# Kernel optimization log

Hardware: AMD Instinct MI355X
Metric: run time of the kernel (lower is better)

## Reference

```python
import jax, jax.numpy as jnp
import numpy as np

B, T, U, V = 4, 300, 80, 1024
DE, DD, INNER = 320, 320, 512


def setup_inputs() -> dict:
    key = jax.random.key(0)
    ks = jax.random.split(key, 6)
    enc_state = jax.random.normal(ks[0], (B, T, DE), jnp.float32)
    dec_state = jax.random.normal(ks[1], (B, U + 1, DD), jnp.float32)
    Wf = jax.random.normal(ks[2], (INNER, DE + DD), jnp.float32) / np.float32(np.sqrt(DE + DD))
    bf = jnp.zeros((INNER,), jnp.float32)
    Wp = jax.random.normal(ks[3], (V, INNER), jnp.float32) / np.float32(np.sqrt(INNER))
    bp = jnp.zeros((V,), jnp.float32)
    targets = jax.random.randint(ks[4], (B, U), 1, V).astype(jnp.int32)  # labels avoid blank=0
    inputs_length = jnp.full((B,), T, jnp.int32)
    targets_length = jnp.full((B,), U, jnp.int32)
    return {"enc_state": enc_state, "dec_state": dec_state, "Wf": Wf, "bf": bf,
            "Wp": Wp, "bp": bp, "targets": targets,
            "inputs_length": inputs_length, "targets_length": targets_length}


def joint_logits(enc, dec, Wf, bf, Wp, bp):
    # Linear over concat([enc, dec]) == Linear(enc) + Linear(dec): avoids materializing the concat.
    de = enc.shape[-1]
    Wf_e, Wf_d = Wf[:, :de], Wf[:, de:]
    enc_p = jnp.einsum('btd,id->bti', enc, Wf_e)   # [B,T,inner]
    dec_p = jnp.einsum('bud,id->bui', dec, Wf_d)   # [B,U1,inner]
    h = jnp.tanh(enc_p[:, :, None, :] + dec_p[:, None, :, :] + bf)  # [B,T,U1,inner]
    return jnp.einsum('btui,vi->btuv', h, Wp) + bp  # [B,T,U1,V]


def rnnt_loss(log_probs, targets, t_len, u_len):
    # log_probs: [B,T,U1,V], blank index 0.
    lp_blank = log_probs[..., 0]  # [B,T,U1]
    lp_emit = jnp.take_along_axis(log_probs[:, :, :-1, :], targets[:, None, :, None], axis=3)[..., 0]  # [B,T,U]
    # row0: alpha[0,u] = sum_{k<u} emit[0,k]
    row0 = jnp.pad(jnp.cumsum(lp_emit[:, 0, :], axis=-1), ((0, 0), (1, 0)))  # [B,U1]

    def outer(alpha_prev, xs):
        blank_prev, emit_cur = xs  # [B,U1], [B,U]
        first = alpha_prev[:, 0] + blank_prev[:, 0]  # [B]

        def inner(c, x):
            a_plus_b, e = x  # [B],[B]
            c2 = jnp.logaddexp(a_plus_b, c + e)
            return c2, c2
        xs_in = ((alpha_prev[:, 1:] + blank_prev[:, 1:]).T, emit_cur.T)  # [U,B]
        _, rest = jax.lax.scan(inner, first, xs_in)  # [U,B]
        row = jnp.concatenate([first[None, :], rest], axis=0).T  # [B,U1]
        return row, row

    xs = (jnp.swapaxes(lp_blank[:, :-1, :], 0, 1), jnp.swapaxes(lp_emit[:, 1:, :], 0, 1))
    _, rows = jax.lax.scan(outer, row0, xs)  # [T-1,B,U1]
    alpha = jnp.concatenate([row0[None], rows], axis=0)  # [T,B,U1]
    bidx = jnp.arange(alpha.shape[1])
    ll = alpha[t_len - 1, bidx, u_len] + lp_blank[bidx, t_len - 1, u_len]
    return -jnp.mean(ll)


def reference(enc_state, dec_state, Wf, bf, Wp, bp, targets, inputs_length, targets_length):
    logits = joint_logits(enc_state, dec_state, Wf, bf, Wp, bp).astype(jnp.float32)
    log_probs = jax.nn.log_softmax(logits, axis=-1)
    return rnnt_loss(log_probs, targets, inputs_length, targets_length)
```

## Files before the change

kernel.cpp:

```cpp
#include <hip/hip_runtime.h>

#define B_DIM 4
#define T_DIM 300
#define U_DIM 80
#define UP1   81
#define V_DIM 1024
#define NINNER 512
#define NROWS (B_DIM * T_DIM * UP1)
#define EP_ROWS (B_DIM * T_DIM)
#define DP_ROWS (B_DIM * UP1)
#define NDIAG 380
#define ZSTR  168
#define ZROWS (B_DIM * NDIAG + 8)
#define WF_PART 163840
#define LOG2E 1.44269504088896341f
#define LN2   0.69314718055994531f
#define NEGF  -1e30f

typedef float f32x4 __attribute__((ext_vector_type(4)));
typedef short short8 __attribute__((ext_vector_type(8)));
typedef short short4v __attribute__((ext_vector_type(4)));
typedef __bf16 bf16x8 __attribute__((ext_vector_type(8)));

static __device__ __forceinline__ short f2bf(float f) {
  return (short)__builtin_bit_cast(unsigned short, (__bf16)f);
}
static __device__ __forceinline__ float bf2f(short s) {
  unsigned int u = ((unsigned int)(unsigned short)s) << 16;
  return __builtin_bit_cast(float, u);
}
static __device__ __forceinline__ float tanh_fast(float x) {
  float e = __builtin_amdgcn_exp2f(x * 2.88539008177792681f);
  return 1.0f - 2.0f * __builtin_amdgcn_rcpf(e + 1.0f);
}
static __device__ __forceinline__ float lse2_2(float a, float b) {
  float mx = fmaxf(a, b), mn = fminf(a, b);
  return mx + __builtin_amdgcn_logf(1.0f + __builtin_amdgcn_exp2f(mn - mx));
}
static __device__ __forceinline__ float ror1f(float x) {
  int r = __builtin_amdgcn_update_dpp(0, __builtin_bit_cast(int, x),
                                      0x13C , 0xF, 0xF, true);
  return __builtin_bit_cast(float, r);
}
static __device__ __forceinline__ float readlanef(float x, int l) {
  return __builtin_bit_cast(float,
      __builtin_amdgcn_readlane(__builtin_bit_cast(int, x), l));
}
static __device__ __forceinline__ f32x4 load4u(const float* p) {
  f32x4 v;
  __builtin_memcpy(&v, p, 16);
  return v;
}

#define CVT_NF 81920
#define CVT_NP 131072
#define FILL_N4 ((ZROWS * ZSTR) / 4)
__global__ __launch_bounds__(256) void cvt_kernel(
    const float* __restrict__ Wf, const float* __restrict__ Wp,
    short* __restrict__ WfB, short* __restrict__ WpB, float* __restrict__ Z) {
  int idx = blockIdx.x * 256 + threadIdx.x;
  if (idx < CVT_NF) {
    float4 v = ((const float4*)Wf)[idx];
    int flat = idx * 4;
    int c = flat / 640;
    int kc = flat - c * 640;
    int part = (kc >= 320);
    int k0 = kc - (part ? 320 : 0);
    int dest = (part ? WF_PART : 0)
             + ((c >> 4) * 10 + (k0 >> 5)) * 512
             + (((k0 >> 3) & 3) * 16 + (c & 15)) * 8 + (k0 & 7);
    short4v o;
    o[0] = f2bf(v.x); o[1] = f2bf(v.y); o[2] = f2bf(v.z); o[3] = f2bf(v.w);
    *(short4v*)(WfB + dest) = o;
  } else if (idx < CVT_NF + CVT_NP) {
    int j = idx - CVT_NF;
    float4 v = ((const float4*)Wp)[j];
    int flat = j * 4;
    int c = flat >> 9;
    int k0 = flat & 511;
    int dest = ((c >> 4) * 16 + (k0 >> 5)) * 512
             + (((k0 >> 3) & 3) * 16 + (c & 15)) * 8 + (k0 & 7);
    short4v o;
    o[0] = f2bf(v.x); o[1] = f2bf(v.y); o[2] = f2bf(v.z); o[3] = f2bf(v.w);
    *(short4v*)(WpB + dest) = o;
  } else {
    int i = idx - (CVT_NF + CVT_NP);
    if (i < FILL_N4) ((f32x4*)Z)[i] = (f32x4){NEGF, NEGF, NEGF, NEGF};
  }
}

#define EP_BLOCKS 19
__global__ __launch_bounds__(256) void proj_kernel(
    const float* __restrict__ enc, const float* __restrict__ dec,
    const short* __restrict__ WfB, const float* __restrict__ bfv,
    short* __restrict__ epB, short* __restrict__ dpB) {
  const int half = blockIdx.x & 1;
  const int ob = blockIdx.x >> 1;
  const bool is_dp = (ob >= EP_BLOCKS);
  const int row0 = (is_dp ? ob - EP_BLOCKS : ob) * 64;
  const int nrows = is_dp ? DP_ROWS : EP_ROWS;
  const float* __restrict__ src = is_dp ? dec : enc;
  const short* __restrict__ bb = WfB + (is_dp ? WF_PART : 0);
  short* __restrict__ out = is_dp ? dpB : epB;

  __shared__ short As[64 * 320];
  const int tid = threadIdx.x;

  #pragma unroll
  for (int it = 0; it < 10; ++it) {
    int chunk = it * 256 + tid;
    int m = chunk / 40;
    int c = chunk - m * 40;
    int r = row0 + m;
    short8 hv;
    #pragma unroll
    for (int j = 0; j < 8; ++j) hv[j] = 0;
    if (r < nrows) {
      const float* p = src + (size_t)r * 320 + c * 8;
      float4 a0 = *(const float4*)p;
      float4 a1 = *(const float4*)(p + 4);
      hv[0] = f2bf(a0.x); hv[1] = f2bf(a0.y); hv[2] = f2bf(a0.z); hv[3] = f2bf(a0.w);
      hv[4] = f2bf(a1.x); hv[5] = f2bf(a1.y); hv[6] = f2bf(a1.z); hv[7] = f2bf(a1.w);
    }
    int off = (m * 640 + c * 16) ^ ((m & 7) << 4);
    *(short8*)((char*)As + off) = hv;
  }
  __syncthreads();

  const int lane = tid & 63, wid = tid >> 6;
  const int lr = lane & 15, g = lane >> 4;

  int lin[4], xm[4];
  #pragma unroll
  for (int mf = 0; mf < 4; ++mf) {
    int row = mf * 16 + lr;
    lin[mf] = row * 640 + g * 16;
    xm[mf] = (row & 7) << 4;
  }

  const int n0 = half * 256 + wid * 64;
  const short* bptr[4];
  float bfc[4];
  #pragma unroll
  for (int nf2 = 0; nf2 < 4; ++nf2) {
    bptr[nf2] = bb + (n0 / 16 + nf2) * 5120 + lane * 8;
    bfc[nf2] = is_dp ? bfv[n0 + nf2 * 16 + lr] : 0.f;
  }
  f32x4 acc[4][4];
  #pragma unroll
  for (int mf = 0; mf < 4; ++mf)
    #pragma unroll
    for (int nf2 = 0; nf2 < 4; ++nf2)
      acc[mf][nf2] = (f32x4){0.f, 0.f, 0.f, 0.f};

  #pragma unroll 2
  for (int kk = 0; kk < 10; ++kk) {
    bf16x8 av[4], bv[4];
    #pragma unroll
    for (int mf = 0; mf < 4; ++mf) {
      int off = (lin[mf] + (kk << 6)) ^ xm[mf];
      av[mf] = __builtin_bit_cast(bf16x8, *(const short8*)((const char*)As + off));
    }
    #pragma unroll
    for (int nf2 = 0; nf2 < 4; ++nf2)
      bv[nf2] = __builtin_bit_cast(bf16x8, *(const short8*)(bptr[nf2] + kk * 512));
    #pragma unroll
    for (int mf = 0; mf < 4; ++mf)
      #pragma unroll
      for (int nf2 = 0; nf2 < 4; ++nf2)
        acc[mf][nf2] = __builtin_amdgcn_mfma_f32_16x16x32_bf16(av[mf], bv[nf2], acc[mf][nf2], 0, 0, 0);
  }
  #pragma unroll
  for (int mf = 0; mf < 4; ++mf)
    #pragma unroll
    for (int nf2 = 0; nf2 < 4; ++nf2)
      #pragma unroll
      for (int rr = 0; rr < 4; ++rr) {
        int rowl = mf * 16 + g * 4 + rr;
        int grow = row0 + rowl;
        if (grow < nrows) {
          int col = n0 + nf2 * 16 + lr;
          out[(size_t)grow * NINNER + col] = f2bf(acc[mf][nf2][rr] + bfc[nf2]);
        }
      }
}

#define JROWS 64
__global__ __launch_bounds__(512) void joint_kernel(
    const short* __restrict__ epB, const short* __restrict__ dpB,
    const short* __restrict__ WpB, const float* __restrict__ bp,
    const int* __restrict__ tgt, float* __restrict__ Z) {
  extern __shared__ char hbuf[];
  __shared__ int ep_off[JROWS], dp_off[JROWS], bld_off[JROWS], eld_off[JROWS], tgt_s[JROWS];
  __shared__ float l0_s[JROWS], lt_s[JROWS];
  __shared__ float ws_s[8][JROWS];

  const int tid = threadIdx.x;
  const int row0 = blockIdx.x * JROWS;

  if (tid < JROWS) {
    int gr = row0 + tid;
    if (gr < NROWS) {
      int b = gr / (T_DIM * UP1);
      int rem = gr - b * (T_DIM * UP1);
      int t = rem / UP1;
      int u = rem - t * UP1;
      ep_off[tid] = (b * T_DIM + t) * NINNER;
      dp_off[tid] = (b * UP1 + u) * NINNER;
      int zrow = (b * NDIAG + (t + u)) * ZSTR;
      bld_off[tid] = zrow + 4 + 2 * u;
      eld_off[tid] = (u < U_DIM) ? (zrow + 4 + 2 * u + 1) : -1;
      tgt_s[tid] = (u < U_DIM) ? tgt[b * U_DIM + u] : 0;
    } else {
      ep_off[tid] = 0; dp_off[tid] = 0; bld_off[tid] = -1; eld_off[tid] = -1; tgt_s[tid] = 0;
    }
    l0_s[tid] = 0.f; lt_s[tid] = 0.f;
  }
  __syncthreads();

  #pragma unroll 2
  for (int it = 0; it < 8; ++it) {
    int chunk = it * 512 + tid;
    int m = chunk >> 6, c = chunk & 63;
    short8 hv;
    #pragma unroll
    for (int j = 0; j < 8; ++j) hv[j] = 0;
    if (bld_off[m] >= 0) {
      short8 ev = *(const short8*)(epB + ep_off[m] + c * 8);
      short8 dv = *(const short8*)(dpB + dp_off[m] + c * 8);
      #pragma unroll
      for (int j = 0; j < 8; ++j)
        hv[j] = f2bf(tanh_fast(bf2f(ev[j]) + bf2f(dv[j])));
    }
    int off = ((m << 10) + (c << 4)) ^ ((m & 7) << 4);
    *(short8*)(hbuf + off) = hv;
  }
  __syncthreads();

  const int lane = tid & 63, wid = tid >> 6;
  const int lr = lane & 15, g = lane >> 4;

  int lin[4], xm[4];
  #pragma unroll
  for (int mf = 0; mf < 4; ++mf) {
    int row = mf * 16 + lr;
    lin[mf] = (row << 10) + (g << 4);
    xm[mf] = (row & 7) << 4;
  }
  int tv[4][4];
  #pragma unroll
  for (int mf = 0; mf < 4; ++mf)
    #pragma unroll
    for (int rr = 0; rr < 4; ++rr)
      tv[mf][rr] = tgt_s[mf * 16 + g * 4 + rr];

  float rsum[4][4];
  #pragma unroll
  for (int mf = 0; mf < 4; ++mf)
    #pragma unroll
    for (int rr = 0; rr < 4; ++rr) rsum[mf][rr] = 0.f;

  #pragma unroll
  for (int sc = 0; sc < 2; ++sc) {
    const int n0 = wid * 128 + sc * 64;
    const short* bptr[4];
    float bpv[4];
    #pragma unroll
    for (int nf = 0; nf < 4; ++nf) {
      bptr[nf] = WpB + (n0 / 16 + nf) * 8192 + lane * 8;
      bpv[nf] = bp[n0 + nf * 16 + lr] * LOG2E;
    }
    f32x4 acc[4][4];
    #pragma unroll
    for (int mf = 0; mf < 4; ++mf)
      #pragma unroll
      for (int nf = 0; nf < 4; ++nf)
        acc[mf][nf] = (f32x4){0.f, 0.f, 0.f, 0.f};

    #pragma unroll 2
    for (int kk = 0; kk < 16; ++kk) {
      bf16x8 av[4], bv[4];
      #pragma unroll
      for (int mf = 0; mf < 4; ++mf) {
        int off = (lin[mf] + (kk << 6)) ^ xm[mf];
        av[mf] = __builtin_bit_cast(bf16x8, *(const short8*)(hbuf + off));
      }
      #pragma unroll
      for (int nf = 0; nf < 4; ++nf)
        bv[nf] = __builtin_bit_cast(bf16x8, *(const short8*)(bptr[nf] + kk * 512));
      __builtin_amdgcn_s_setprio(1);
      #pragma unroll
      for (int mf = 0; mf < 4; ++mf)
        #pragma unroll
        for (int nf = 0; nf < 4; ++nf)
          acc[mf][nf] = __builtin_amdgcn_mfma_f32_16x16x32_bf16(av[mf], bv[nf], acc[mf][nf], 0, 0, 0);
      __builtin_amdgcn_s_setprio(0);
    }
    #pragma unroll
    for (int mf = 0; mf < 4; ++mf)
      #pragma unroll
      for (int rr = 0; rr < 4; ++rr) {
        float x0 = __builtin_fmaf(acc[mf][0][rr], LOG2E, bpv[0]);
        float x1 = __builtin_fmaf(acc[mf][1][rr], LOG2E, bpv[1]);
        float x2 = __builtin_fmaf(acc[mf][2][rr], LOG2E, bpv[2]);
        float x3 = __builtin_fmaf(acc[mf][3][rr], LOG2E, bpv[3]);
        int rowl = mf * 16 + g * 4 + rr;
        if (wid == 0 && sc == 0 && lr == 0) l0_s[rowl] = x0;
        int dtv = tv[mf][rr] - n0;
        if (dtv >= 0 && dtv < 64 && (dtv & 15) == lr) {
          int nfi = dtv >> 4;
          lt_s[rowl] = (nfi == 0) ? x0 : (nfi == 1) ? x1 : (nfi == 2) ? x2 : x3;
        }
        rsum[mf][rr] += __builtin_amdgcn_exp2f(x0) + __builtin_amdgcn_exp2f(x1)
                      + __builtin_amdgcn_exp2f(x2) + __builtin_amdgcn_exp2f(x3);
      }
  }
  #pragma unroll
  for (int mf = 0; mf < 4; ++mf)
    #pragma unroll
    for (int rr = 0; rr < 4; ++rr) {
      float s_ = rsum[mf][rr];
      #pragma unroll
      for (int o = 1; o < 16; o <<= 1) s_ += __shfl_xor(s_, o);
      if (lr == 0) ws_s[wid][mf * 16 + g * 4 + rr] = s_;
    }
  __syncthreads();
  if (tid < JROWS) {
    int bo = bld_off[tid];
    if (bo >= 0) {
      float S = 0.f;
      #pragma unroll
      for (int w = 0; w < 8; ++w) S += ws_s[w][tid];
      float lse2v = __builtin_amdgcn_logf(S);
      Z[bo] = l0_s[tid] - lse2v;
      int eo = eld_off[tid];
      if (eo >= 0) Z[eo] = lt_s[tid] - lse2v;
    }
  }
}

#define ACH 8
#define NCH 48
__global__ __launch_bounds__(256) void alpha_kernel(
    const float* __restrict__ Z,
    const int* __restrict__ ilen, const int* __restrict__ ulen_,
    float* __restrict__ out) {
  __shared__ float lls[B_DIM];
  const int tid = threadIdx.x;
  const int b = tid >> 6;
  const int lane = tid & 63;
  const float NEG = NEGF;
  const int tl = ilen[b], ul = ulen_[b];
  const int dstar = tl - 1 + ul;

  const int u0 = lane;
  const int u1 = 64 + lane;
  const bool act1 = (u1 <= 80);
  const int uc1 = act1 ? u1 : 80;

  const float* Zb = Z + (size_t)b * (NDIAG * ZSTR);

  f32x4 Aq0[ACH], Aq1[ACH], Bq0[ACH], Bq1[ACH];

  #define ALOAD(P, c)                                                        \
    {                                                                        \
      const float* base0 = Zb + (c) * (ACH * ZSTR) + 1 + 2 * u0;             \
      const float* base1 = Zb + (c) * (ACH * ZSTR) + 1 + 2 * uc1;            \
      _Pragma("unroll")                                                      \
      for (int j = 0; j < ACH; ++j) {                                        \
        P##q0[j] = load4u(base0 + j * ZSTR);                                 \
        P##q1[j] = load4u(base1 + j * ZSTR);                                 \
      }                                                                      \
    }

  #define ACOMP(P, c)                                                        \
    {                                                                        \
      _Pragma("unroll")                                                      \
      for (int q = 0; q < ACH / 2; ++q) {                                    \
        const int j = 2 * q;                                                 \
        const int s1 = (c) * ACH + j + 1;                                    \
                                    \
        float a63 = readlanef(pa0, 63), a62 = readlanef(pa0, 62);            \
        float s0m1 = ror1f(pa0);                                             \
        float s0m2 = ror1f(s0m1);                                            \
        float s1m1r = ror1f(pa1);                                            \
        float s1m2r = ror1f(s1m1r);                                          \
        float s1m1 = (lane == 0) ? a63 : s1m1r;                              \
        float s1m2 = (lane == 0) ? a62 : ((lane == 1) ? a63 : s1m2r);        \
        float na0, na1;                                                      \
        {                        \
          f32x4 v = P##q0[j], w = P##q0[j + 1];                              \
          float T1 = v[3] + w[3];                                            \
          float T2 = lse2_2(v[2] + w[3], v[1] + w[2]);                       \
          float T3 = v[0] + w[2];                                            \
          float p0 = pa0 + T1;                                               \
          float p1 = s0m1 + T2;                                              \
          float p2 = s0m2 + T3;                                              \
          float mx = fmaxf(fmaxf(p0, p1), p2);                               \
          float ss = __builtin_amdgcn_exp2f(p0 - mx)                         \
                   + __builtin_amdgcn_exp2f(p1 - mx)                         \
                   + __builtin_amdgcn_exp2f(p2 - mx);                        \
          na0 = fmaxf(mx + __builtin_amdgcn_logf(ss), NEG);                  \
        }                                                                    \
        {                                                        \
          f32x4 v = P##q1[j], w = P##q1[j + 1];                              \
          float T1 = v[3] + w[3];                                            \
          float T2 = lse2_2(v[2] + w[3], v[1] + w[2]);                       \
          float T3 = v[0] + w[2];                                            \
          float p0 = pa1 + T1;                                               \
          float p1 = s1m1 + T2;                                              \
          float p2 = s1m2 + T3;                                              \
          float mx = fmaxf(fmaxf(p0, p1), p2);                               \
          float ss = __builtin_amdgcn_exp2f(p0 - mx)                         \
                   + __builtin_amdgcn_exp2f(p1 - mx)                         \
                   + __builtin_amdgcn_exp2f(p2 - mx);                        \
          na1 = fmaxf(mx + __builtin_amdgcn_logf(ss), NEG);                  \
        }                                                                    \
        if (s1 == dstar) {                   \
          float vo0 = lse2_2(pa0 + P##q0[j][3], s0m1 + P##q0[j][2]);         \
          if (u0 == ul) fin = vo0;                                           \
          float vo1 = lse2_2(pa1 + P##q1[j][3], s1m1 + P##q1[j][2]);         \
          if (act1 && u1 == ul) fin = vo1;                                   \
        }                                                                    \
        pa0 = na0; pa1 = na1;                                                \
        if (s1 + 1 == dstar) {              \
          if (u0 == ul) fin = pa0;                                           \
          if (act1 && u1 == ul) fin = pa1;                                   \
        }                                                                    \
      }                                                                      \
    }

  float pa0 = (u0 == 0) ? 0.f : NEG;
  float pa1 = NEG;
  float fin = NEG;
  if (dstar == 0 && u0 == ul) fin = pa0;

  ALOAD(A, 0);
  for (int p = 0; p < NCH / 2; ++p) {
    const int cA = 2 * p, cB = 2 * p + 1;
    ALOAD(B, cB);
    ACOMP(A, cA);
    ALOAD(A, cA + 2);
    ACOMP(B, cB);
  }

  #pragma unroll
  for (int o = 32; o; o >>= 1) fin = fmaxf(fin, __shfl_xor(fin, o));
  if (lane == 0) {
    float last = Zb[(size_t)dstar * ZSTR + 4 + 2 * ul];
    lls[b] = fin + last;
  }
  __syncthreads();
  if (tid == 0)
    out[0] = -(lls[0] + lls[1] + lls[2] + lls[3]) * (LN2 * 0.25f);
}

extern "C" void kernel_launch(void* const* d_in, const int* in_sizes, int n_in,
                              void* d_out, int out_size, void* d_ws, size_t ws_size,
                              hipStream_t stream) {
  const float* enc = (const float*)d_in[0];
  const float* dec = (const float*)d_in[1];
  const float* Wf  = (const float*)d_in[2];
  const float* bfv = (const float*)d_in[3];
  const float* Wp  = (const float*)d_in[4];
  const float* bp  = (const float*)d_in[5];
  const int* targets = (const int*)d_in[6];
  const int* ilen    = (const int*)d_in[7];
  const int* ulen    = (const int*)d_in[8];
  float* out = (float*)d_out;
  char* ws = (char*)d_ws;

  short* WfB = (short*)(ws + 0);
  short* WpB = (short*)(ws + 655360);
  short* epB = (short*)(ws + 1703936);
  short* dpB = (short*)(ws + 2932736);
  float* Z   = (float*)(ws + 3264512);

  cvt_kernel<<<1083, 256, 0, stream>>>(Wf, Wp, WfB, WpB, Z);
  proj_kernel<<<50, 256, 0, stream>>>(enc, dec, WfB, bfv, epB, dpB);
  joint_kernel<<<(NROWS + JROWS - 1) / JROWS, 512, 65536, stream>>>(epB, dpB, WpB, bp, targets, Z);
  alpha_kernel<<<1, 256, 0, stream>>>(Z, ilen, ulen, out);
}
```

Baseline: 198.9 us.

## Pipeline tanh hidden-tile construction with first-half MFMA k-loop

Builds the bf16 tanh hidden tile in four k-chunks instead of all at once before the GEMM. The next chunk's global loads are issued during the current chunk's MFMAs for the first 64-column block, then tanh'd and written with a barrier per chunk. The second column block runs separately on the full tile. This hides load and tanh latency behind matrix work, but adds three barriers, more live registers, and removes the masking of invalid rows (bld_off<0) and the setprio hints.

```diff
diff --git a/kernel.cpp b/kernel.cpp
--- a/kernel.cpp
+++ b/kernel.cpp
@@ -218,23 +218,38 @@
   }
   __syncthreads();
 
-  #pragma unroll 2
-  for (int it = 0; it < 8; ++it) {
-    int chunk = it * 512 + tid;
-    int m = chunk >> 6, c = chunk & 63;
-    short8 hv;
-    #pragma unroll
-    for (int j = 0; j < 8; ++j) hv[j] = 0;
-    if (bld_off[m] >= 0) {
-      short8 ev = *(const short8*)(epB + ep_off[m] + c * 8);
-      short8 dv = *(const short8*)(dpB + dp_off[m] + c * 8);
-      #pragma unroll
-      for (int j = 0; j < 8; ++j)
-        hv[j] = f2bf(tanh_fast(bf2f(ev[j]) + bf2f(dv[j])));
-    }
-    int off = ((m << 10) + (c << 4)) ^ ((m & 7) << 4);
-    *(short8*)(hbuf + off) = hv;
-  }
+  const int m0 = tid >> 4;
+  const int m1 = 32 + m0;
+  const int cq = tid & 15;
+  const short* pe0 = epB + ep_off[m0] + cq * 8;
+  const short* pd0 = dpB + dp_off[m0] + cq * 8;
+  const short* pe1 = epB + ep_off[m1] + cq * 8;
+  const short* pd1 = dpB + dp_off[m1] + cq * 8;
+  const int po0 = ((m0 << 10) + (cq << 4)) ^ ((m0 & 7) << 4);
+  const int po1 = ((m1 << 10) + (cq << 4)) ^ ((m1 & 7) << 4);
+
+  short8 sev0, sdv0, sev1, sdv1;
+#define STAGE_LOAD(q)                                  \
+  {                                                    \
+    sev0 = *(const short8*)(pe0 + (q) * 128);          \
+    sdv0 = *(const short8*)(pd0 + (q) * 128);          \
+    sev1 = *(const short8*)(pe1 + (q) * 128);          \
+    sdv1 = *(const short8*)(pd1 + (q) * 128);          \
+  }
+#define STAGE_WRITE(q)                                                \
+  {                                                                   \
+    short8 h0, h1;                                                    \
+    _Pragma("unroll")                                                 \
+    for (int j = 0; j < 8; ++j) {                                     \
+      h0[j] = f2bf(tanh_fast(bf2f(sev0[j]) + bf2f(sdv0[j])));         \
+      h1[j] = f2bf(tanh_fast(bf2f(sev1[j]) + bf2f(sdv1[j])));         \
+    }                                                                 \
+    *(short8*)(hbuf + po0 + (q) * 256) = h0;                          \
+    *(short8*)(hbuf + po1 + (q) * 256) = h1;                          \
+  }
+
+  STAGE_LOAD(0)
+  STAGE_WRITE(0)
   __syncthreads();
 
   const int lane = tid & 63, wid = tid >> 6;
@@ -260,9 +275,8 @@
     #pragma unroll
     for (int rr = 0; rr < 4; ++rr) rsum[mf][rr] = 0.f;
 
-  #pragma unroll
-  for (int sc = 0; sc < 2; ++sc) {
-    const int n0 = wid * 128 + sc * 64;
+  {
+    const int n0 = wid * 128;
     const short* bptr[4];
     float bpv[4];
     #pragma unroll
@@ -277,24 +291,31 @@
       for (int nf = 0; nf < 4; ++nf)
         acc[mf][nf] = (f32x4){0.f, 0.f, 0.f, 0.f};
 
-    #pragma unroll 2
-    for (int kk = 0; kk < 16; ++kk) {
-      bf16x8 av[4], bv[4];
-      #pragma unroll
-      for (int mf = 0; mf < 4; ++mf) {
-        int off = (lin[mf] + (kk << 6)) ^ xm[mf];
-        av[mf] = __builtin_bit_cast(bf16x8, *(const short8*)(hbuf + off));
-      }
-      #pragma unroll
-      for (int nf = 0; nf < 4; ++nf)
-        bv[nf] = __builtin_bit_cast(bf16x8, *(const short8*)(bptr[nf] + kk * 512));
-      __builtin_amdgcn_s_setprio(1);
-      #pragma unroll
-      for (int mf = 0; mf < 4; ++mf)
+    #pragma unroll
+    for (int qq = 0; qq < 4; ++qq) {
+      if (qq < 3) STAGE_LOAD(qq + 1)
+      #pragma unroll
+      for (int i = 0; i < 4; ++i) {
+        const int kk = qq * 4 + i;
+        bf16x8 av[4], bv[4];
+        #pragma unroll
+        for (int mf = 0; mf < 4; ++mf) {
+          int off = (lin[mf] + (kk << 6)) ^ xm[mf];
+          av[mf] = __builtin_bit_cast(bf16x8, *(const short8*)(hbuf + off));
+        }
         #pragma unroll
         for (int nf = 0; nf < 4; ++nf)
-          acc[mf][nf] = __builtin_amdgcn_mfma_f32_16x16x32_bf16(av[mf], bv[nf], acc[mf][nf], 0, 0, 0);
-      __builtin_amdgcn_s_setprio(0);
+          bv[nf] = __builtin_bit_cast(bf16x8, *(const short8*)(bptr[nf] + kk * 512));
+        #pragma unroll
+        for (int mf = 0; mf < 4; ++mf)
+          #pragma unroll
+          for (int nf = 0; nf < 4; ++nf)
+            acc[mf][nf] = __builtin_amdgcn_mfma_f32_16x16x32_bf16(av[mf], bv[nf], acc[mf][nf], 0, 0, 0);
+      }
+      if (qq < 3) {
+        STAGE_WRITE(qq + 1)
+        __syncthreads();
+      }
     }
     #pragma unroll
     for (int mf = 0; mf < 4; ++mf)
@@ -305,7 +326,7 @@
         float x2 = __builtin_fmaf(acc[mf][2][rr], LOG2E, bpv[2]);
         float x3 = __builtin_fmaf(acc[mf][3][rr], LOG2E, bpv[3]);
         int rowl = mf * 16 + g * 4 + rr;
-        if (wid == 0 && sc == 0 && lr == 0) l0_s[rowl] = x0;
+        if (wid == 0 && lr == 0) l0_s[rowl] = x0;
         int dtv = tv[mf][rr] - n0;
         if (dtv >= 0 && dtv < 64 && (dtv & 15) == lr) {
           int nfi = dtv >> 4;
@@ -315,6 +336,59 @@
                       + __builtin_amdgcn_exp2f(x2) + __builtin_amdgcn_exp2f(x3);
       }
   }
+
+  {
+    const int n0 = wid * 128 + 64;
+    const short* bptr[4];
+    float bpv[4];
+    #pragma unroll
+    for (int nf = 0; nf < 4; ++nf) {
+      bptr[nf] = WpB + (n0 / 16 + nf) * 8192 + lane * 8;
+      bpv[nf] = bp[n0 + nf * 16 + lr] * LOG2E;
+    }
+    f32x4 acc[4][4];
+    #pragma unroll
+    for (int mf = 0; mf < 4; ++mf)
+      #pragma unroll
+      for (int nf = 0; nf < 4; ++nf)
+        acc[mf][nf] = (f32x4){0.f, 0.f, 0.f, 0.f};
+
+    #pragma unroll 2
+    for (int kk = 0; kk < 16; ++kk) {
+      bf16x8 av[4], bv[4];
+      #pragma unroll
+      for (int mf = 0; mf < 4; ++mf) {
+        int off = (lin[mf] + (kk << 6)) ^ xm[mf];
+        av[mf] = __builtin_bit_cast(bf16x8, *(const short8*)(hbuf + off));
+      }
+      #pragma unroll
+      for (int nf = 0; nf < 4; ++nf)
+        bv[nf] = __builtin_bit_cast(bf16x8, *(const short8*)(bptr[nf] + kk * 512));
+      #pragma unroll
+      for (int mf = 0; mf < 4; ++mf)
+        #pragma unroll
+        for (int nf = 0; nf < 4; ++nf)
+          acc[mf][nf] = __builtin_amdgcn_mfma_f32_16x16x32_bf16(av[mf], bv[nf], acc[mf][nf], 0, 0, 0);
+    }
+    #pragma unroll
+    for (int mf = 0; mf < 4; ++mf)
+      #pragma unroll
+      for (int rr = 0; rr < 4; ++rr) {
+        float x0 = __builtin_fmaf(acc[mf][0][rr], LOG2E, bpv[0]);
+        float x1 = __builtin_fmaf(acc[mf][1][rr], LOG2E, bpv[1]);
+        float x2 = __builtin_fmaf(acc[mf][2][rr], LOG2E, bpv[2]);
+        float x3 = __builtin_fmaf(acc[mf][3][rr], LOG2E, bpv[3]);
+        int rowl = mf * 16 + g * 4 + rr;
+        int dtv = tv[mf][rr] - n0;
+        if (dtv >= 0 && dtv < 64 && (dtv & 15) == lr) {
+          int nfi = dtv >> 4;
+          lt_s[rowl] = (nfi == 0) ? x0 : (nfi == 1) ? x1 : (nfi == 2) ? x2 : x3;
+        }
+        rsum[mf][rr] += __builtin_amdgcn_exp2f(x0) + __builtin_amdgcn_exp2f(x1)
+                      + __builtin_amdgcn_exp2f(x2) + __builtin_amdgcn_exp2f(x3);
+      }
+  }
+
   #pragma unroll
   for (int mf = 0; mf < 4; ++mf)
     #pragma unroll
```

Result: faster. 190.8 us (-4.1%).

## Double row tile in joint kernel and overlap tanh staging with MFMA

Applied to the files above, without the earlier changes.

The joint kernel tile grows from 64 to 128 rows, so each Wp fragment loaded from global memory feeds twice as many MFMAs. The tanh(enc+dec) hidden tile is now built in four K-chunks, and each chunk's global loads are issued while the MFMAs of the previous chunk run. The aim is to cut Wp global traffic per row and hide the hidden-tile build latency. In exchange, shared memory doubles to 128KB and the accumulator array doubles to 128 floats per thread, which lowers occupancy and adds register pressure and extra barriers.

```diff
diff --git a/kernel.cpp b/kernel.cpp
--- a/kernel.cpp
+++ b/kernel.cpp
@@ -185,7 +185,7 @@
       }
 }
 
-#define JROWS 64
+#define JROWS 128
 __global__ __launch_bounds__(512) void joint_kernel(
     const short* __restrict__ epB, const short* __restrict__ dpB,
     const short* __restrict__ WpB, const float* __restrict__ bp,
@@ -218,86 +218,91 @@
   }
   __syncthreads();
 
-  #pragma unroll 2
-  for (int it = 0; it < 8; ++it) {
-    int chunk = it * 512 + tid;
-    int m = chunk >> 6, c = chunk & 63;
-    short8 hv;
-    #pragma unroll
-    for (int j = 0; j < 8; ++j) hv[j] = 0;
-    if (bld_off[m] >= 0) {
-      short8 ev = *(const short8*)(epB + ep_off[m] + c * 8);
-      short8 dv = *(const short8*)(dpB + dp_off[m] + c * 8);
-      #pragma unroll
-      for (int j = 0; j < 8; ++j)
-        hv[j] = f2bf(tanh_fast(bf2f(ev[j]) + bf2f(dv[j])));
-    }
-    int off = ((m << 10) + (c << 4)) ^ ((m & 7) << 4);
-    *(short8*)(hbuf + off) = hv;
-  }
+  const int m0 = tid >> 4;
+  const int cq = tid & 15;
+  int eoff[4], doff[4], po[4];
+  #pragma unroll
+  for (int r = 0; r < 4; ++r) {
+    int m = m0 + r * 32;
+    eoff[r] = ep_off[m] + cq * 8;
+    doff[r] = dp_off[m] + cq * 8;
+    po[r] = ((m << 10) + (cq << 4)) ^ ((m & 7) << 4);
+  }
+
+  short8 sev[4], sdv[4];
+#define STAGE_LOAD(q)                                         \
+  {                                                           \
+    _Pragma("unroll")                                         \
+    for (int r = 0; r < 4; ++r) {                             \
+      sev[r] = *(const short8*)(epB + eoff[r] + (q) * 128);   \
+      sdv[r] = *(const short8*)(dpB + doff[r] + (q) * 128);   \
+    }                                                         \
+  }
+#define STAGE_WRITE(q)                                                  \
+  {                                                                     \
+    _Pragma("unroll")                                                   \
+    for (int r = 0; r < 4; ++r) {                                       \
+      short8 h;                                                         \
+      _Pragma("unroll")                                                 \
+      for (int j = 0; j < 8; ++j)                                       \
+        h[j] = f2bf(tanh_fast(bf2f(sev[r][j]) + bf2f(sdv[r][j])));      \
+      *(short8*)(hbuf + po[r] + (q) * 256) = h;                         \
+    }                                                                   \
+  }
+
+  STAGE_LOAD(0)
+  STAGE_WRITE(0)
   __syncthreads();
 
   const int lane = tid & 63, wid = tid >> 6;
   const int lr = lane & 15, g = lane >> 4;
 
-  int lin[4], xm[4];
-  #pragma unroll
-  for (int mf = 0; mf < 4; ++mf) {
-    int row = mf * 16 + lr;
-    lin[mf] = (row << 10) + (g << 4);
-    xm[mf] = (row & 7) << 4;
-  }
-  int tv[4][4];
-  #pragma unroll
-  for (int mf = 0; mf < 4; ++mf)
-    #pragma unroll
-    for (int rr = 0; rr < 4; ++rr)
-      tv[mf][rr] = tgt_s[mf * 16 + g * 4 + rr];
-
-  float rsum[4][4];
-  #pragma unroll
-  for (int mf = 0; mf < 4; ++mf)
-    #pragma unroll
-    for (int rr = 0; rr < 4; ++rr) rsum[mf][rr] = 0.f;
+  const int lin0 = (lr << 10) + (g << 4);
+  const int xm = (lr & 7) << 4;
 
   #pragma unroll
   for (int sc = 0; sc < 2; ++sc) {
     const int n0 = wid * 128 + sc * 64;
-    const short* bptr[4];
+    int boff[4];
     float bpv[4];
     #pragma unroll
     for (int nf = 0; nf < 4; ++nf) {
-      bptr[nf] = WpB + (n0 / 16 + nf) * 8192 + lane * 8;
+      boff[nf] = (n0 / 16 + nf) * 8192 + lane * 8;
       bpv[nf] = bp[n0 + nf * 16 + lr] * LOG2E;
     }
-    f32x4 acc[4][4];
-    #pragma unroll
-    for (int mf = 0; mf < 4; ++mf)
+    f32x4 acc[8][4];
+    #pragma unroll
+    for (int mf = 0; mf < 8; ++mf)
       #pragma unroll
       for (int nf = 0; nf < 4; ++nf)
         acc[mf][nf] = (f32x4){0.f, 0.f, 0.f, 0.f};
 
-    #pragma unroll 2
-    for (int kk = 0; kk < 16; ++kk) {
-      bf16x8 av[4], bv[4];
-      #pragma unroll
-      for (int mf = 0; mf < 4; ++mf) {
-        int off = (lin[mf] + (kk << 6)) ^ xm[mf];
-        av[mf] = __builtin_bit_cast(bf16x8, *(const short8*)(hbuf + off));
-      }
-      #pragma unroll
-      for (int nf = 0; nf < 4; ++nf)
-        bv[nf] = __builtin_bit_cast(bf16x8, *(const short8*)(bptr[nf] + kk * 512));
-      __builtin_amdgcn_s_setprio(1);
-      #pragma unroll
-      for (int mf = 0; mf < 4; ++mf)
+    #pragma unroll
+    for (int qq = 0; qq < 4; ++qq) {
+      if (sc == 0 && qq < 3) STAGE_LOAD(qq + 1)
+      #pragma unroll
+      for (int i = 0; i < 4; ++i) {
+        const int kk = qq * 4 + i;
+        bf16x8 bv[4];
         #pragma unroll
         for (int nf = 0; nf < 4; ++nf)
-          acc[mf][nf] = __builtin_amdgcn_mfma_f32_16x16x32_bf16(av[mf], bv[nf], acc[mf][nf], 0, 0, 0);
-      __builtin_amdgcn_s_setprio(0);
-    }
-    #pragma unroll
-    for (int mf = 0; mf < 4; ++mf)
+          bv[nf] = __builtin_bit_cast(bf16x8, *(const short8*)(WpB + boff[nf] + kk * 512));
+        #pragma unroll
+        for (int mf = 0; mf < 8; ++mf) {
+          int off = (lin0 + mf * 16384 + (kk << 6)) ^ xm;
+          bf16x8 av = __builtin_bit_cast(bf16x8, *(const short8*)(hbuf + off));
+          #pragma unroll
+          for (int nf = 0; nf < 4; ++nf)
+            acc[mf][nf] = __builtin_amdgcn_mfma_f32_16x16x32_bf16(av, bv[nf], acc[mf][nf], 0, 0, 0);
+        }
+      }
+      if (sc == 0 && qq < 3) {
+        STAGE_WRITE(qq + 1)
+        __syncthreads();
+      }
+    }
+    #pragma unroll
+    for (int mf = 0; mf < 8; ++mf)
       #pragma unroll
       for (int rr = 0; rr < 4; ++rr) {
         float x0 = __builtin_fmaf(acc[mf][0][rr], LOG2E, bpv[0]);
@@ -306,24 +311,21 @@
         float x3 = __builtin_fmaf(acc[mf][3][rr], LOG2E, bpv[3]);
         int rowl = mf * 16 + g * 4 + rr;
         if (wid == 0 && sc == 0 && lr == 0) l0_s[rowl] = x0;
-        int dtv = tv[mf][rr] - n0;
+        int dtv = tgt_s[rowl] - n0;
         if (dtv >= 0 && dtv < 64 && (dtv & 15) == lr) {
           int nfi = dtv >> 4;
           lt_s[rowl] = (nfi == 0) ? x0 : (nfi == 1) ? x1 : (nfi == 2) ? x2 : x3;
         }
-        rsum[mf][rr] += __builtin_amdgcn_exp2f(x0) + __builtin_amdgcn_exp2f(x1)
-                      + __builtin_amdgcn_exp2f(x2) + __builtin_amdgcn_exp2f(x3);
+        float s_ = __builtin_amdgcn_exp2f(x0) + __builtin_amdgcn_exp2f(x1)
+                 + __builtin_amdgcn_exp2f(x2) + __builtin_amdgcn_exp2f(x3);
+        #pragma unroll
+        for (int o = 1; o < 16; o <<= 1) s_ += __shfl_xor(s_, o);
+        if (lr == 0) {
+          if (sc == 0) ws_s[wid][rowl] = s_;
+          else         ws_s[wid][rowl] += s_;
+        }
       }
   }
-  #pragma unroll
-  for (int mf = 0; mf < 4; ++mf)
-    #pragma unroll
-    for (int rr = 0; rr < 4; ++rr) {
-      float s_ = rsum[mf][rr];
-      #pragma unroll
-      for (int o = 1; o < 16; o <<= 1) s_ += __shfl_xor(s_, o);
-      if (lr == 0) ws_s[wid][mf * 16 + g * 4 + rr] = s_;
-    }
   __syncthreads();
   if (tid < JROWS) {
     int bo = bld_off[tid];
@@ -478,6 +480,6 @@
 
   cvt_kernel<<<1083, 256, 0, stream>>>(Wf, Wp, WfB, WpB, Z);
   proj_kernel<<<50, 256, 0, stream>>>(enc, dec, WfB, bfv, epB, dpB);
-  joint_kernel<<<(NROWS + JROWS - 1) / JROWS, 512, 65536, stream>>>(epB, dpB, WpB, bp, targets, Z);
+  joint_kernel<<<(NROWS + JROWS - 1) / JROWS, 512, 131072, stream>>>(epB, dpB, WpB, bp, targets, Z);
   alpha_kernel<<<1, 256, 0, stream>>>(Z, ilen, ulen, out);
 }
```

After: 259.8 us. 1.31x slower.

## Switch joint GEMM to FP8 MFMA and pipeline tanh staging with compute

Applied to the files above, without the earlier changes.

Converts Wp and the tanh hidden activations to FP8 (e4m3) and uses the fp8 16x16x32 MFMA instead of bf16, halving LDS footprint and weight bandwidth. The hidden tile is now built in four K-quarters that are loaded and written between MFMA chunks of the first N pass, overlapping global loads and tanh with matrix work. LDS usage drops from 64KB to 32KB, which may allow more blocks per CU. The cost is lower precision in the logits feeding log-softmax and the loss, plus extra barriers inside the loop.

```diff
diff --git a/kernel.cpp b/kernel.cpp
--- a/kernel.cpp
+++ b/kernel.cpp
@@ -21,6 +21,7 @@
 typedef short short8 __attribute__((ext_vector_type(8)));
 typedef short short4v __attribute__((ext_vector_type(4)));
 typedef __bf16 bf16x8 __attribute__((ext_vector_type(8)));
+typedef int int2v __attribute__((ext_vector_type(2)));
 
 static __device__ __forceinline__ short f2bf(float f) {
   return (short)__builtin_bit_cast(unsigned short, (__bf16)f);
@@ -50,6 +51,15 @@
   f32x4 v;
   __builtin_memcpy(&v, p, 16);
   return v;
+}
+static __device__ __forceinline__ long load8(const void* p) {
+  long v;
+  __builtin_memcpy(&v, p, 8);
+  return v;
+}
+template <bool HI>
+static __device__ __forceinline__ int pkf8(float a, float b, int old) {
+  return __builtin_amdgcn_cvt_pk_fp8_f32(a, b, old, HI);
 }
 
 #define CVT_NF 81920
@@ -57,7 +67,7 @@
 #define FILL_N4 ((ZROWS * ZSTR) / 4)
 __global__ __launch_bounds__(256) void cvt_kernel(
     const float* __restrict__ Wf, const float* __restrict__ Wp,
-    short* __restrict__ WfB, short* __restrict__ WpB, float* __restrict__ Z) {
+    short* __restrict__ WfB, char* __restrict__ WpB8, float* __restrict__ Z) {
   int idx = blockIdx.x * 256 + threadIdx.x;
   if (idx < CVT_NF) {
     float4 v = ((const float4*)Wf)[idx];
@@ -80,9 +90,9 @@
     int k0 = flat & 511;
     int dest = ((c >> 4) * 16 + (k0 >> 5)) * 512
              + (((k0 >> 3) & 3) * 16 + (c & 15)) * 8 + (k0 & 7);
-    short4v o;
-    o[0] = f2bf(v.x); o[1] = f2bf(v.y); o[2] = f2bf(v.z); o[3] = f2bf(v.w);
-    *(short4v*)(WpB + dest) = o;
+    int w = pkf8<false>(v.x, v.y, 0);
+    w = pkf8<true>(v.z, v.w, w);
+    *(int*)(WpB8 + dest) = w;
   } else {
     int i = idx - (CVT_NF + CVT_NP);
     if (i < FILL_N4) ((f32x4*)Z)[i] = (f32x4){NEGF, NEGF, NEGF, NEGF};
@@ -188,7 +198,7 @@
 #define JROWS 64
 __global__ __launch_bounds__(512) void joint_kernel(
     const short* __restrict__ epB, const short* __restrict__ dpB,
-    const short* __restrict__ WpB, const float* __restrict__ bp,
+    const char* __restrict__ WpB8, const float* __restrict__ bp,
     const int* __restrict__ tgt, float* __restrict__ Z) {
   extern __shared__ char hbuf[];
   __shared__ int ep_off[JROWS], dp_off[JROWS], bld_off[JROWS], eld_off[JROWS], tgt_s[JROWS];
@@ -218,35 +228,53 @@
   }
   __syncthreads();
 
-  #pragma unroll 2
-  for (int it = 0; it < 8; ++it) {
-    int chunk = it * 512 + tid;
-    int m = chunk >> 6, c = chunk & 63;
-    short8 hv;
-    #pragma unroll
-    for (int j = 0; j < 8; ++j) hv[j] = 0;
-    if (bld_off[m] >= 0) {
-      short8 ev = *(const short8*)(epB + ep_off[m] + c * 8);
-      short8 dv = *(const short8*)(dpB + dp_off[m] + c * 8);
-      #pragma unroll
-      for (int j = 0; j < 8; ++j)
-        hv[j] = f2bf(tanh_fast(bf2f(ev[j]) + bf2f(dv[j])));
-    }
-    int off = ((m << 10) + (c << 4)) ^ ((m & 7) << 4);
-    *(short8*)(hbuf + off) = hv;
-  }
+  const int m0 = tid >> 4;
+  const int m1 = 32 + m0;
+  const int cq = tid & 15;
+  const short* pe0 = epB + ep_off[m0] + cq * 8;
+  const short* pd0 = dpB + dp_off[m0] + cq * 8;
+  const short* pe1 = epB + ep_off[m1] + cq * 8;
+  const short* pd1 = dpB + dp_off[m1] + cq * 8;
+  const int po0 = ((m0 << 9) + (cq << 3)) ^ ((m0 & 7) << 3);
+  const int po1 = ((m1 << 9) + (cq << 3)) ^ ((m1 & 7) << 3);
+
+  short8 sev0, sdv0, sev1, sdv1;
+#define STAGE_LOAD(q)                                  \
+  {                                                    \
+    sev0 = *(const short8*)(pe0 + (q) * 128);          \
+    sdv0 = *(const short8*)(pd0 + (q) * 128);          \
+    sev1 = *(const short8*)(pe1 + (q) * 128);          \
+    sdv1 = *(const short8*)(pd1 + (q) * 128);          \
+  }
+#define STAGE_WRITE(q)                                                    \
+  {                                                                       \
+    float h0[8], h1[8];                                                   \
+    _Pragma("unroll")                                                     \
+    for (int j = 0; j < 8; ++j) {                                         \
+      h0[j] = tanh_fast(bf2f(sev0[j]) + bf2f(sdv0[j]));                   \
+      h1[j] = tanh_fast(bf2f(sev1[j]) + bf2f(sdv1[j]));                   \
+    }                                                                     \
+    int2v w0, w1;                                                         \
+    w0[0] = pkf8<true>(h0[2], h0[3], pkf8<false>(h0[0], h0[1], 0));       \
+    w0[1] = pkf8<true>(h0[6], h0[7], pkf8<false>(h0[4], h0[5], 0));       \
+    w1[0] = pkf8<true>(h1[2], h1[3], pkf8<false>(h1[0], h1[1], 0));       \
+    w1[1] = pkf8<true>(h1[6], h1[7], pkf8<false>(h1[4], h1[5], 0));       \
+    *(int2v*)(hbuf + po0 + (q) * 128) = w0;                               \
+    *(int2v*)(hbuf + po1 + (q) * 128) = w1;                               \
+  }
+
+  STAGE_LOAD(0)
+  STAGE_WRITE(0)
   __syncthreads();
 
   const int lane = tid & 63, wid = tid >> 6;
   const int lr = lane & 15, g = lane >> 4;
 
-  int lin[4], xm[4];
-  #pragma unroll
-  for (int mf = 0; mf < 4; ++mf) {
-    int row = mf * 16 + lr;
-    lin[mf] = (row << 10) + (g << 4);
-    xm[mf] = (row & 7) << 4;
-  }
+  int lin[4];
+  #pragma unroll
+  for (int mf = 0; mf < 4; ++mf)
+    lin[mf] = ((mf * 16 + lr) << 9) + (g << 3);
+  const int xm = (lr & 7) << 3;
   int tv[4][4];
   #pragma unroll
   for (int mf = 0; mf < 4; ++mf)
@@ -263,11 +291,11 @@
   #pragma unroll
   for (int sc = 0; sc < 2; ++sc) {
     const int n0 = wid * 128 + sc * 64;
-    const short* bptr[4];
+    const char* bptr[4];
     float bpv[4];
     #pragma unroll
     for (int nf = 0; nf < 4; ++nf) {
-      bptr[nf] = WpB + (n0 / 16 + nf) * 8192 + lane * 8;
+      bptr[nf] = WpB8 + (n0 / 16 + nf) * 8192 + lane * 8;
       bpv[nf] = bp[n0 + nf * 16 + lr] * LOG2E;
     }
     f32x4 acc[4][4];
@@ -277,24 +305,31 @@
       for (int nf = 0; nf < 4; ++nf)
         acc[mf][nf] = (f32x4){0.f, 0.f, 0.f, 0.f};
 
-    #pragma unroll 2
-    for (int kk = 0; kk < 16; ++kk) {
-      bf16x8 av[4], bv[4];
-      #pragma unroll
-      for (int mf = 0; mf < 4; ++mf) {
-        int off = (lin[mf] + (kk << 6)) ^ xm[mf];
-        av[mf] = __builtin_bit_cast(bf16x8, *(const short8*)(hbuf + off));
-      }
-      #pragma unroll
-      for (int nf = 0; nf < 4; ++nf)
-        bv[nf] = __builtin_bit_cast(bf16x8, *(const short8*)(bptr[nf] + kk * 512));
-      __builtin_amdgcn_s_setprio(1);
-      #pragma unroll
-      for (int mf = 0; mf < 4; ++mf)
+    #pragma unroll
+    for (int qq = 0; qq < 4; ++qq) {
+      if (sc == 0 && qq < 3) STAGE_LOAD(qq + 1)
+      #pragma unroll
+      for (int i = 0; i < 4; ++i) {
+        const int kk = qq * 4 + i;
+        long av[4], bv[4];
+        #pragma unroll
+        for (int mf = 0; mf < 4; ++mf) {
+          int off = ((lin[mf] + ((kk & 3) << 5)) ^ xm) + ((kk >> 2) << 7);
+          av[mf] = load8(hbuf + off);
+        }
         #pragma unroll
         for (int nf = 0; nf < 4; ++nf)
-          acc[mf][nf] = __builtin_amdgcn_mfma_f32_16x16x32_bf16(av[mf], bv[nf], acc[mf][nf], 0, 0, 0);
-      __builtin_amdgcn_s_setprio(0);
+          bv[nf] = load8(bptr[nf] + kk * 512);
+        #pragma unroll
+        for (int mf = 0; mf < 4; ++mf)
+          #pragma unroll
+          for (int nf = 0; nf < 4; ++nf)
+            acc[mf][nf] = __builtin_amdgcn_mfma_f32_16x16x32_fp8_fp8(av[mf], bv[nf], acc[mf][nf], 0, 0, 0);
+      }
+      if (sc == 0 && qq < 3) {
+        STAGE_WRITE(qq + 1)
+        __syncthreads();
+      }
     }
     #pragma unroll
     for (int mf = 0; mf < 4; ++mf)
@@ -470,14 +505,14 @@
   float* out = (float*)d_out;
   char* ws = (char*)d_ws;
 
-  short* WfB = (short*)(ws + 0);
-  short* WpB = (short*)(ws + 655360);
-  short* epB = (short*)(ws + 1703936);
-  short* dpB = (short*)(ws + 2932736);
-  float* Z   = (float*)(ws + 3264512);
-
-  cvt_kernel<<<1083, 256, 0, stream>>>(Wf, Wp, WfB, WpB, Z);
+  short* WfB  = (short*)(ws + 0);
+  char*  WpB8 = (char*)(ws + 655360);
+  short* epB  = (short*)(ws + 1179648);
+  short* dpB  = (short*)(ws + 2408448);
+  float* Z    = (float*)(ws + 2740224);
+
+  cvt_kernel<<<1083, 256, 0, stream>>>(Wf, Wp, WfB, WpB8, Z);
   proj_kernel<<<50, 256, 0, stream>>>(enc, dec, WfB, bfv, epB, dpB);
-  joint_kernel<<<(NROWS + JROWS - 1) / JROWS, 512, 65536, stream>>>(epB, dpB, WpB, bp, targets, Z);
+  joint_kernel<<<(NROWS + JROWS - 1) / JROWS, 512, 32768, stream>>>(epB, dpB, WpB8, bp, targets, Z);
   alpha_kernel<<<1, 256, 0, stream>>>(Z, ilen, ulen, out);
 }
```

Measured after the change: 186.7 us (median of 2 runs). 6.1% less time.
